# Performance work log

Hardware: AMD Instinct MI355X
Metric: run time of the kernel (lower is better)

The kernel has to match this reference:

```python
import jax, jax.numpy as jnp
import numpy as np

N_NODES = 50000
N_EDGES = 800000
N_GRAPHS = 64
IN_DIM, HID, OUT = 128, 128, 16


def gcn_conv(x, src, dst, deg_inv_sqrt, W, b):
    # x: [N, Cin]; src/dst: [E+N] (self-loops appended); W: [Cin, Cout]
    h = x @ W                                   # [N, Cout]
    norm = deg_inv_sqrt[src] * deg_inv_sqrt[dst]  # [E+N]
    msg = h[src] * norm[:, None]                # gather + scale
    out = jax.ops.segment_sum(msg, dst, num_segments=N_NODES)
    return out + b


def setup_inputs() -> dict:
    key = jax.random.key(0)
    ks = jax.random.split(key, 8)
    x = jax.random.normal(ks[0], (N_NODES, IN_DIM), dtype=jnp.float32)
    edge_index = jax.random.randint(ks[1], (2, N_EDGES), 0, N_NODES, dtype=jnp.int64)
    batch = jnp.sort(jax.random.randint(ks[2], (N_NODES,), 0, N_GRAPHS, dtype=jnp.int64))
    s = 1.0 / np.sqrt(IN_DIM)
    W1 = jax.random.normal(ks[3], (IN_DIM, HID), dtype=jnp.float32) * s
    b1 = jnp.zeros((HID,), dtype=jnp.float32)
    W2 = jax.random.normal(ks[4], (HID, HID), dtype=jnp.float32) * (1.0 / np.sqrt(HID))
    b2 = jnp.zeros((HID,), dtype=jnp.float32)
    Wfc = jax.random.normal(ks[5], (HID, OUT), dtype=jnp.float32) * (1.0 / np.sqrt(HID))
    bfc = jnp.zeros((OUT,), dtype=jnp.float32)
    return {"x": x, "edge_index": edge_index, "batch": batch,
            "W1": W1, "b1": b1, "W2": W2, "b2": b2, "Wfc": Wfc, "bfc": bfc}


def reference(x, edge_index, batch, W1, b1, W2, b2, Wfc, bfc):
    self_loops = jnp.arange(N_NODES, dtype=edge_index.dtype)
    src = jnp.concatenate([edge_index[0], self_loops])  # [E+N]
    dst = jnp.concatenate([edge_index[1], self_loops])
    deg = jax.ops.segment_sum(jnp.ones_like(dst, dtype=x.dtype), dst, num_segments=N_NODES)
    deg_inv_sqrt = jnp.where(deg > 0, jax.lax.rsqrt(deg), 0.0)

    h = jax.nn.relu(gcn_conv(x, src, dst, deg_inv_sqrt, W1, b1))
    h = jax.nn.relu(gcn_conv(h, src, dst, deg_inv_sqrt, W2, b2))

    # global mean pool over graphs
    sums = jax.ops.segment_sum(h, batch, num_segments=N_GRAPHS)         # [G, HID]
    cnts = jax.ops.segment_sum(jnp.ones((N_NODES,), h.dtype), batch, num_segments=N_GRAPHS)
    pooled = sums / jnp.maximum(cnts, 1.0)[:, None]

    return pooled @ Wfc + bfc  # [G, OUT]
```

## Files before the change

kernel.cpp:

```cpp
#include <hip/hip_runtime.h>
#include <math.h>

#define N_NODES 50000
#define N_EDGES 800000
#define N_GRAPHS 64
#define DIM 128
#define OUTD 16
#define POOL_BLOCKS 1024

#define BSHIFT 8
#define BNODES 256
#define NBUCK ((N_NODES + BNODES - 1) / BNODES)
#define TILE 2048
#define RCAP 8192
#define BSLOT 4864
#define GEMMB 256
#define BIN_GRID ((N_EDGES + TILE - 1) / TILE)

typedef __attribute__((ext_vector_type(8))) short short8;
typedef __attribute__((ext_vector_type(4))) float f32x4;

static __device__ __forceinline__ unsigned short f2bf(float f) {
    unsigned u = __float_as_uint(f);
    u += 0x7fffu + ((u >> 16) & 1u);
    return (unsigned short)(u >> 16);
}
static __device__ __forceinline__ float bfl(unsigned u) {
    return __uint_as_float(u << 16);
}
static __device__ __forceinline__ float bfh(unsigned u) {
    return __uint_as_float(u & 0xffff0000u);
}
static __device__ __forceinline__ float b2f(unsigned short u) {
    return __uint_as_float((unsigned)u << 16);
}

__global__ __launch_bounds__(256) void k_init(int* __restrict__ bcnt,
                                              float* __restrict__ pool,
                                              float* __restrict__ pcnt) {
    int tid = threadIdx.x;
    if (tid < NBUCK) bcnt[tid] = 0;
    for (int i = tid; i < N_GRAPHS * DIM; i += 256) pool[i] = 0.f;
    if (tid < N_GRAPHS) pcnt[tid] = 0.f;
}

template <int BF16IN>
static __device__ __forceinline__ void gemm_body(const void* __restrict__ Av,
                                                 const float* __restrict__ Wg,
                                                 unsigned short* __restrict__ C,
                                                 int nrows,
                                                 unsigned* smemW, unsigned* smemC,
                                                 int tile0, int tstride) {
    unsigned* Wl = smemW;
    {
        int t = threadIdx.x;
        int p = t & 63;
        int kp = p * 2;
        int n0 = (t >> 6) * 32;
        int kstep = kp >> 5;
        int quad = (kp >> 3) & 3;
        int jw = (kp & 7) >> 1;
        const float* r0 = Wg + (size_t)kp * DIM;
        const float* r1 = r0 + DIM;
        int rot = (p >> 2) & 7;
#pragma unroll
        for (int i4 = 0; i4 < 8; ++i4) {
            int nb = ((i4 + rot) & 7) * 4;
            int n = n0 + nb;
            float4 lo = *(const float4*)(r0 + n);
            float4 hi = *(const float4*)(r1 + n);
            const float* lp = &lo.x;
            const float* hp = &hi.x;
#pragma unroll
            for (int ii = 0; ii < 4; ++ii) {
                int nn = n + ii;
                int ct = nn >> 4;
                int l  = quad * 16 + (nn & 15);
                unsigned vlo = f2bf(lp[ii]);
                unsigned vhi = f2bf(hp[ii]);
                Wl[(((kstep * 8 + ct) * 64) + l) * 4 + jw] = vlo | (vhi << 16);
            }
        }
    }
    __syncthreads();

    int wid  = threadIdx.x >> 6;
    int lane = threadIdx.x & 63;
    int m    = lane & 15;
    int quad = lane >> 4;
    const short8* Wf = (const short8*)Wl;
    unsigned short* cs = (unsigned short*)smemC + wid * 4352;
    const unsigned char* cb = (const unsigned char*)smemC + wid * 8704;

    int ntiles = (nrows + 127) / 128;
    for (int tile = tile0; tile < ntiles; tile += tstride) {
        int row0 = tile * 128 + wid * 32;
        if (row0 >= nrows) continue;

        int rA = row0 + m;      if (rA >= nrows) rA = nrows - 1;
        int rB = row0 + 16 + m; if (rB >= nrows) rB = nrows - 1;

        short8 af0[4], af1[4];
        if (BF16IN) {
            const unsigned short* arowA = (const unsigned short*)Av + (size_t)rA * DIM + quad * 8;
            const unsigned short* arowB = (const unsigned short*)Av + (size_t)rB * DIM + quad * 8;
#pragma unroll
            for (int ks = 0; ks < 4; ++ks) {
                af0[ks] = *(const short8*)(arowA + ks * 32);
                af1[ks] = *(const short8*)(arowB + ks * 32);
            }
        } else {
            const float* arowA = (const float*)Av + (size_t)rA * DIM + quad * 8;
            const float* arowB = (const float*)Av + (size_t)rB * DIM + quad * 8;
#pragma unroll
            for (int ks = 0; ks < 4; ++ks) {
                float4 lo = *(const float4*)(arowA + ks * 32);
                float4 hi = *(const float4*)(arowA + ks * 32 + 4);
                short8 f;
                f[0] = (short)f2bf(lo.x); f[1] = (short)f2bf(lo.y);
                f[2] = (short)f2bf(lo.z); f[3] = (short)f2bf(lo.w);
                f[4] = (short)f2bf(hi.x); f[5] = (short)f2bf(hi.y);
                f[6] = (short)f2bf(hi.z); f[7] = (short)f2bf(hi.w);
                af0[ks] = f;
                lo = *(const float4*)(arowB + ks * 32);
                hi = *(const float4*)(arowB + ks * 32 + 4);
                f[0] = (short)f2bf(lo.x); f[1] = (short)f2bf(lo.y);
                f[2] = (short)f2bf(lo.z); f[3] = (short)f2bf(lo.w);
                f[4] = (short)f2bf(hi.x); f[5] = (short)f2bf(hi.y);
                f[6] = (short)f2bf(hi.z); f[7] = (short)f2bf(hi.w);
                af1[ks] = f;
            }
        }

        f32x4 acc0[8], acc1[8];
#pragma unroll
        for (int ct = 0; ct < 8; ++ct) {
            acc0[ct] = (f32x4){0.f, 0.f, 0.f, 0.f};
            acc1[ct] = (f32x4){0.f, 0.f, 0.f, 0.f};
        }

#pragma unroll
        for (int ks = 0; ks < 4; ++ks) {
#pragma unroll
            for (int ct = 0; ct < 8; ++ct) {
                short8 bfrag = Wf[(ks * 8 + ct) * 64 + lane];
                acc0[ct] = __builtin_amdgcn_mfma_f32_16x16x32_bf16(af0[ks], bfrag, acc0[ct], 0, 0, 0);
                acc1[ct] = __builtin_amdgcn_mfma_f32_16x16x32_bf16(af1[ks], bfrag, acc1[ct], 0, 0, 0);
            }
        }

#pragma unroll
        for (int ct = 0; ct < 8; ++ct) {
#pragma unroll
            for (int reg = 0; reg < 4; ++reg) {
                cs[(quad * 4 + reg) * 136 + ct * 16 + m]      = f2bf(acc0[ct][reg]);
                cs[(16 + quad * 4 + reg) * 136 + ct * 16 + m] = f2bf(acc1[ct][reg]);
            }
        }
#pragma unroll
        for (int i = 0; i < 8; ++i) {
            int rg = i * 4 + quad;
            int r = row0 + rg;
            if (r < nrows) {
                uint4 vv = *(const uint4*)(cb + rg * 272 + m * 16);
                *((uint4*)(C + (size_t)r * DIM) + m) = vv;
            }
        }
    }
}

__global__ __launch_bounds__(256) void k_fused1(const float* __restrict__ A,
                                                const float* __restrict__ Wg,
                                                unsigned short* __restrict__ C,
                                                int nrows,
                                                const int* __restrict__ src,
                                                const int* __restrict__ dstp,
                                                int* __restrict__ bcnt,
                                                unsigned* __restrict__ bucket_arr) {
    __shared__ unsigned smemW[32768 / 4];
    __shared__ unsigned smemC[34816 / 4];
    if (blockIdx.x >= GEMMB) {
        int* cnt  = (int*)smemW;
        int* base = cnt + NBUCK;
        int tile0 = (blockIdx.x - GEMMB) * TILE;
        for (int i = threadIdx.x; i < NBUCK; i += 256) cnt[i] = 0;
        __syncthreads();
#pragma unroll
        for (int j = 0; j < TILE / 512; ++j) {
            int e = tile0 + j * 512 + threadIdx.x * 2;
            if (e < N_EDGES) {
                int2 d = *(const int2*)(dstp + e);
                atomicAdd(&cnt[d.x >> BSHIFT], 1);
                atomicAdd(&cnt[d.y >> BSHIFT], 1);
            }
        }
        __syncthreads();
        for (int i = threadIdx.x; i < NBUCK; i += 256) {
            int c = cnt[i];
            base[i] = i * BSLOT + (c ? atomicAdd(&bcnt[i], c) : 0);
            cnt[i] = 0;
        }
        __syncthreads();
#pragma unroll
        for (int j = 0; j < TILE / 512; ++j) {
            int e = tile0 + j * 512 + threadIdx.x * 2;
            if (e < N_EDGES) {
                int2 s = *(const int2*)(src + e);
                int2 d = *(const int2*)(dstp + e);
                int b0 = d.x >> BSHIFT, b1 = d.y >> BSHIFT;
                int p0 = base[b0] + atomicAdd(&cnt[b0], 1);
                bucket_arr[p0] = (unsigned)s.x | ((unsigned)(d.x & 255) << 16);
                int p1 = base[b1] + atomicAdd(&cnt[b1], 1);
                bucket_arr[p1] = (unsigned)s.y | ((unsigned)(d.y & 255) << 16);
            }
        }
        return;
    }
    gemm_body<0>(A, Wg, C, nrows, smemW, smemC, blockIdx.x, GEMMB);
}

__global__ __launch_bounds__(256) void k_gemm2(const unsigned short* __restrict__ A,
                                               const float* __restrict__ Wg,
                                               unsigned short* __restrict__ C,
                                               int nrows) {
    __shared__ unsigned smemW[32768 / 4];
    __shared__ unsigned smemC[34816 / 4];
    gemm_body<1>(A, Wg, C, nrows, smemW, smemC, blockIdx.x, gridDim.x);
}

__global__ __launch_bounds__(256) void k_binB(const unsigned* __restrict__ barr,
                                              const int* __restrict__ bcnt,
                                              int* __restrict__ row_off,
                                              float* __restrict__ dis,
                                              unsigned short* __restrict__ csr) {
    __shared__ unsigned raw[RCAP];
    __shared__ unsigned short stage[RCAP];
    __shared__ int hist[BNODES];
    __shared__ int scn[BNODES];
    __shared__ int borig[256], bscan[256];
    int tid = threadIdx.x;
    int b = blockIdx.x;
    int n0 = b << BSHIFT;

    int cv = (tid < NBUCK) ? bcnt[tid] : 0;
    borig[tid] = cv;
    bscan[tid] = cv;
    __syncthreads();
    for (int off = 1; off < 256; off <<= 1) {
        int t = (tid >= off) ? bscan[tid - off] : 0;
        __syncthreads();
        bscan[tid] += t;
        __syncthreads();
    }
    int rbase = bscan[b] - borig[b];
    int len = borig[b];
    const unsigned* bin = barr + (size_t)b * BSLOT;

    hist[tid] = 0;
    __syncthreads();
    for (int i = tid; i < len; i += 256) {
        unsigned ed = bin[i];
        if (i < RCAP) raw[i] = ed;
        atomicAdd(&hist[ed >> 16], 1);
    }
    __syncthreads();
    int v = hist[tid];
    scn[tid] = v;
    __syncthreads();
    for (int off = 1; off < 256; off <<= 1) {
        int t = (tid >= off) ? scn[tid - off] : 0;
        __syncthreads();
        scn[tid] += t;
        __syncthreads();
    }
    int excl = scn[tid] - v;
    int n = n0 + tid;
    if (n < N_NODES) {
        row_off[n] = rbase + excl;
        dis[n] = rsqrtf((float)(v + 1));
    }
    if (b == NBUCK - 1 && tid == 0) row_off[N_NODES] = N_EDGES;
    hist[tid] = excl;
    __syncthreads();
    for (int i = tid; i < len; i += 256) {
        unsigned ed = (i < RCAP) ? raw[i] : bin[i];
        int p = atomicAdd(&hist[ed >> 16], 1);
        unsigned short sv = (unsigned short)(ed & 0xffffu);
        if (p < RCAP) stage[p] = sv;
        else csr[rbase + p] = sv;
    }
    __syncthreads();
    int lim = min(len, RCAP);
    for (int i = tid; i < lim; i += 256)
        csr[rbase + i] = stage[i];
}

__global__ __launch_bounds__(256) void k_agg(const uint4* __restrict__ Hb4,
                                             const int* __restrict__ row_off,
                                             const unsigned short* __restrict__ csr,
                                             const float* __restrict__ dis,
                                             const float* __restrict__ bias,
                                             uint4* __restrict__ out) {
    int lane = threadIdx.x & 15;
    int node = blockIdx.x * 16 + (threadIdx.x >> 4);
    if (node >= N_NODES) return;

    float dn = dis[node];
    float wself = dn * dn;
    uint4 hp = Hb4[(size_t)node * 16 + lane];
    float a0[8], a1[8], a2[8], a3[8];
    a0[0] = wself * bfl(hp.x); a0[1] = wself * bfh(hp.x);
    a0[2] = wself * bfl(hp.y); a0[3] = wself * bfh(hp.y);
    a0[4] = wself * bfl(hp.z); a0[5] = wself * bfh(hp.z);
    a0[6] = wself * bfl(hp.w); a0[7] = wself * bfh(hp.w);
#pragma unroll
    for (int j = 0; j < 8; ++j) { a1[j] = 0.f; a2[j] = 0.f; a3[j] = 0.f; }

    int e = row_off[node], e1 = row_off[node + 1];
    for (; e + 4 <= e1; e += 4) {
        int s0 = csr[e];     int s1 = csr[e + 1];
        int s2 = csr[e + 2]; int s3 = csr[e + 3];
        uint4 g0 = Hb4[(size_t)s0 * 16 + lane];
        uint4 g1 = Hb4[(size_t)s1 * 16 + lane];
        uint4 g2 = Hb4[(size_t)s2 * 16 + lane];
        uint4 g3 = Hb4[(size_t)s3 * 16 + lane];
        float w0 = dn * dis[s0], w1 = dn * dis[s1];
        float w2 = dn * dis[s2], w3 = dn * dis[s3];
        a0[0] = fmaf(w0, bfl(g0.x), a0[0]); a0[1] = fmaf(w0, bfh(g0.x), a0[1]);
        a0[2] = fmaf(w0, bfl(g0.y), a0[2]); a0[3] = fmaf(w0, bfh(g0.y), a0[3]);
        a0[4] = fmaf(w0, bfl(g0.z), a0[4]); a0[5] = fmaf(w0, bfh(g0.z), a0[5]);
        a0[6] = fmaf(w0, bfl(g0.w), a0[6]); a0[7] = fmaf(w0, bfh(g0.w), a0[7]);
        a1[0] = fmaf(w1, bfl(g1.x), a1[0]); a1[1] = fmaf(w1, bfh(g1.x), a1[1]);
        a1[2] = fmaf(w1, bfl(g1.y), a1[2]); a1[3] = fmaf(w1, bfh(g1.y), a1[3]);
        a1[4] = fmaf(w1, bfl(g1.z), a1[4]); a1[5] = fmaf(w1, bfh(g1.z), a1[5]);
        a1[6] = fmaf(w1, bfl(g1.w), a1[6]); a1[7] = fmaf(w1, bfh(g1.w), a1[7]);
        a2[0] = fmaf(w2, bfl(g2.x), a2[0]); a2[1] = fmaf(w2, bfh(g2.x), a2[1]);
        a2[2] = fmaf(w2, bfl(g2.y), a2[2]); a2[3] = fmaf(w2, bfh(g2.y), a2[3]);
        a2[4] = fmaf(w2, bfl(g2.z), a2[4]); a2[5] = fmaf(w2, bfh(g2.z), a2[5]);
        a2[6] = fmaf(w2, bfl(g2.w), a2[6]); a2[7] = fmaf(w2, bfh(g2.w), a2[7]);
        a3[0] = fmaf(w3, bfl(g3.x), a3[0]); a3[1] = fmaf(w3, bfh(g3.x), a3[1]);
        a3[2] = fmaf(w3, bfl(g3.y), a3[2]); a3[3] = fmaf(w3, bfh(g3.y), a3[3]);
        a3[4] = fmaf(w3, bfl(g3.z), a3[4]); a3[5] = fmaf(w3, bfh(g3.z), a3[5]);
        a3[6] = fmaf(w3, bfl(g3.w), a3[6]); a3[7] = fmaf(w3, bfh(g3.w), a3[7]);
    }
    for (; e < e1; ++e) {
        int s = csr[e];
        uint4 g = Hb4[(size_t)s * 16 + lane];
        float w = dn * dis[s];
        a0[0] = fmaf(w, bfl(g.x), a0[0]); a0[1] = fmaf(w, bfh(g.x), a0[1]);
        a0[2] = fmaf(w, bfl(g.y), a0[2]); a0[3] = fmaf(w, bfh(g.y), a0[3]);
        a0[4] = fmaf(w, bfl(g.z), a0[4]); a0[5] = fmaf(w, bfh(g.z), a0[5]);
        a0[6] = fmaf(w, bfl(g.w), a0[6]); a0[7] = fmaf(w, bfh(g.w), a0[7]);
    }

    float4 b0 = ((const float4*)bias)[lane * 2];
    float4 b1v = ((const float4*)bias)[lane * 2 + 1];
    float r[8];
    r[0] = fmaxf(a0[0] + a1[0] + a2[0] + a3[0] + b0.x, 0.f);
    r[1] = fmaxf(a0[1] + a1[1] + a2[1] + a3[1] + b0.y, 0.f);
    r[2] = fmaxf(a0[2] + a1[2] + a2[2] + a3[2] + b0.z, 0.f);
    r[3] = fmaxf(a0[3] + a1[3] + a2[3] + a3[3] + b0.w, 0.f);
    r[4] = fmaxf(a0[4] + a1[4] + a2[4] + a3[4] + b1v.x, 0.f);
    r[5] = fmaxf(a0[5] + a1[5] + a2[5] + a3[5] + b1v.y, 0.f);
    r[6] = fmaxf(a0[6] + a1[6] + a2[6] + a3[6] + b1v.z, 0.f);
    r[7] = fmaxf(a0[7] + a1[7] + a2[7] + a3[7] + b1v.w, 0.f);
    uint4 ov;
    ov.x = (unsigned)f2bf(r[0]) | ((unsigned)f2bf(r[1]) << 16);
    ov.y = (unsigned)f2bf(r[2]) | ((unsigned)f2bf(r[3]) << 16);
    ov.z = (unsigned)f2bf(r[4]) | ((unsigned)f2bf(r[5]) << 16);
    ov.w = (unsigned)f2bf(r[6]) | ((unsigned)f2bf(r[7]) << 16);
    out[(size_t)node * 16 + lane] = ov;
}

__global__ __launch_bounds__(128) void k_pool(const unsigned short* __restrict__ h,
                                              const int* __restrict__ batch,
                                              float* __restrict__ pool,
                                              float* __restrict__ pcnt) {
    int chunk = (N_NODES + POOL_BLOCKS - 1) / POOL_BLOCKS;
    int n0 = blockIdx.x * chunk;
    int n1 = min(n0 + chunk, N_NODES);
    if (n0 >= n1) return;
    int c = threadIdx.x;
    int curg = batch[n0];
    float acc = 0.f;
    int count = 0;
    int n = n0;
    for (; n + 4 <= n1; ) {
        int g0 = batch[n], g3 = batch[n + 3];
        if (g0 == curg && g3 == curg) {
            float v0 = b2f(h[(size_t)(n + 0) * DIM + c]);
            float v1 = b2f(h[(size_t)(n + 1) * DIM + c]);
            float v2 = b2f(h[(size_t)(n + 2) * DIM + c]);
            float v3 = b2f(h[(size_t)(n + 3) * DIM + c]);
            acc += (v0 + v1) + (v2 + v3);
            count += 4;
            n += 4;
        } else {
            int g = g0;
            if (g != curg) {
                atomicAdd(&pool[curg * DIM + c], acc);
                if (c == 0) atomicAdd(&pcnt[curg], (float)count);
                acc = 0.f; count = 0; curg = g;
            }
            acc += b2f(h[(size_t)n * DIM + c]);
            count++;
            n += 1;
        }
    }
    for (; n < n1; ++n) {
        int g = batch[n];
        if (g != curg) {
            atomicAdd(&pool[curg * DIM + c], acc);
            if (c == 0) atomicAdd(&pcnt[curg], (float)count);
            acc = 0.f; count = 0; curg = g;
        }
        acc += b2f(h[(size_t)n * DIM + c]);
        count++;
    }
    atomicAdd(&pool[curg * DIM + c], acc);
    if (c == 0) atomicAdd(&pcnt[curg], (float)count);
}

__global__ void k_fc(const float* __restrict__ pool, const float* __restrict__ pcnt,
                     const float* __restrict__ Wfc, const float* __restrict__ bfc,
                     float* __restrict__ out) {
    int id = blockIdx.x * blockDim.x + threadIdx.x;
    if (id >= N_GRAPHS * OUTD) return;
    int g = id >> 4, o = id & 15;
    float inv = 1.0f / fmaxf(pcnt[g], 1.0f);
    float acc = bfc[o];
    const float* p = pool + g * DIM;
    for (int c = 0; c < DIM; ++c)
        acc = fmaf(p[c] * inv, Wfc[c * OUTD + o], acc);
    out[id] = acc;
}


extern "C" void kernel_launch(void* const* d_in, const int* in_sizes, int n_in,
                              void* d_out, int out_size, void* d_ws, size_t ws_size,
                              hipStream_t stream) {
    const float* x    = (const float*)d_in[0];
    const int*   ei   = (const int*)d_in[1];
    const int*   batch= (const int*)d_in[2];
    const float* W1   = (const float*)d_in[3];
    const float* b1   = (const float*)d_in[4];
    const float* W2   = (const float*)d_in[5];
    const float* b2   = (const float*)d_in[6];
    const float* Wfc  = (const float*)d_in[7];
    const float* bfc  = (const float*)d_in[8];
    float* out = (float*)d_out;

    char* ws = (char*)d_ws;
    size_t off = 0;
    auto alloc = [&](size_t bytes) -> char* {
        char* p = ws + off;
        off = (off + bytes + 255) & ~(size_t)255;
        return p;
    };
    int*      bcnt     = (int*)     alloc((size_t)NBUCK * 4);
    int*      row_off  = (int*)     alloc((size_t)(N_NODES + 1) * 4);
    float*    dis      = (float*)   alloc((size_t)N_NODES * 4);
    unsigned short* csr= (unsigned short*)alloc((size_t)N_EDGES * 2);
    unsigned* barr     = (unsigned*)alloc((size_t)NBUCK * BSLOT * 4);
    float*    pool     = (float*)   alloc((size_t)N_GRAPHS * DIM * 4);
    float*    pcnt     = (float*)   alloc((size_t)N_GRAPHS * 4);
    unsigned short* Hb = (unsigned short*)alloc((size_t)N_NODES * DIM * 2);
    unsigned short* Hb2= (unsigned short*)alloc((size_t)N_NODES * DIM * 2);

    const int* src = ei;
    const int* dst = ei + N_EDGES;

    k_init<<<1, 256, 0, stream>>>(bcnt, pool, pcnt);
    k_fused1<<<GEMMB + BIN_GRID, 256, 0, stream>>>(x, W1, Hb, N_NODES,
                                                   src, dst, bcnt, barr);
    k_binB<<<NBUCK, 256, 0, stream>>>(barr, bcnt, row_off, dis, csr);

    int agg_grid = (N_NODES + 15) / 16;
    k_agg<<<agg_grid, 256, 0, stream>>>((const uint4*)Hb, row_off, csr, dis, b1, (uint4*)Hb2);
    k_gemm2<<<GEMMB, 256, 0, stream>>>(Hb2, W2, Hb, N_NODES);
    k_agg<<<agg_grid, 256, 0, stream>>>((const uint4*)Hb, row_off, csr, dis, b2, (uint4*)Hb2);
    k_pool<<<POOL_BLOCKS, DIM, 0, stream>>>(Hb2, batch, pool, pcnt);
    k_fc<<<(N_GRAPHS * OUTD + 255) / 256, 256, 0, stream>>>(pool, pcnt, Wfc, bfc, out);
}
```

Before: 207.9 us.

## Fuse global mean pooling into second aggregation and derive graph counts by binary search

The second aggregation kernel now reduces each block's 16 node rows in shared memory, per graph id. It then atomically adds the partial sums into the pooled buffer, instead of writing the bf16 hidden state and running a separate pool kernel. Per-graph node counts are now computed in the final FC kernel by binary search over the sorted batch array, which removes the count atomics and the count buffer. This avoids a full write and re-read of the second-layer activations and one kernel launch. In exchange there are many more global float atomics on the small pool buffer, and a block-level barrier in the aggregation kernel.

```diff
diff --git a/kernel.cpp b/kernel.cpp
--- a/kernel.cpp
+++ b/kernel.cpp
@@ -6,7 +6,6 @@
 #define N_GRAPHS 64
 #define DIM 128
 #define OUTD 16
-#define POOL_BLOCKS 1024
 
 #define BSHIFT 8
 #define BNODES 256
@@ -31,17 +30,12 @@
 static __device__ __forceinline__ float bfh(unsigned u) {
     return __uint_as_float(u & 0xffff0000u);
 }
-static __device__ __forceinline__ float b2f(unsigned short u) {
-    return __uint_as_float((unsigned)u << 16);
-}
 
 __global__ __launch_bounds__(256) void k_init(int* __restrict__ bcnt,
-                                              float* __restrict__ pool,
-                                              float* __restrict__ pcnt) {
+                                              float* __restrict__ pool) {
     int tid = threadIdx.x;
     if (tid < NBUCK) bcnt[tid] = 0;
     for (int i = tid; i < N_GRAPHS * DIM; i += 256) pool[i] = 0.f;
-    if (tid < N_GRAPHS) pcnt[tid] = 0.f;
 }
 
 template <int BF16IN>
@@ -295,14 +289,20 @@
         csr[rbase + i] = stage[i];
 }
 
+template <int FUSE_POOL>
 __global__ __launch_bounds__(256) void k_agg(const uint4* __restrict__ Hb4,
                                              const int* __restrict__ row_off,
                                              const unsigned short* __restrict__ csr,
                                              const float* __restrict__ dis,
                                              const float* __restrict__ bias,
-                                             uint4* __restrict__ out) {
+                                             uint4* __restrict__ out,
+                                             const int* __restrict__ batch,
+                                             float* __restrict__ pool) {
+    __shared__ float sacc[16][DIM];
+    __shared__ int sg[16];
     int lane = threadIdx.x & 15;
-    int node = blockIdx.x * 16 + (threadIdx.x >> 4);
+    int nl   = threadIdx.x >> 4;
+    int node = blockIdx.x * 16 + nl;
     if (node >= N_NODES) return;
 
     float dn = dis[node];
@@ -364,70 +364,50 @@
     r[5] = fmaxf(a0[5] + a1[5] + a2[5] + a3[5] + b1v.y, 0.f);
     r[6] = fmaxf(a0[6] + a1[6] + a2[6] + a3[6] + b1v.z, 0.f);
     r[7] = fmaxf(a0[7] + a1[7] + a2[7] + a3[7] + b1v.w, 0.f);
-    uint4 ov;
-    ov.x = (unsigned)f2bf(r[0]) | ((unsigned)f2bf(r[1]) << 16);
-    ov.y = (unsigned)f2bf(r[2]) | ((unsigned)f2bf(r[3]) << 16);
-    ov.z = (unsigned)f2bf(r[4]) | ((unsigned)f2bf(r[5]) << 16);
-    ov.w = (unsigned)f2bf(r[6]) | ((unsigned)f2bf(r[7]) << 16);
-    out[(size_t)node * 16 + lane] = ov;
-}
-
-__global__ __launch_bounds__(128) void k_pool(const unsigned short* __restrict__ h,
-                                              const int* __restrict__ batch,
-                                              float* __restrict__ pool,
-                                              float* __restrict__ pcnt) {
-    int chunk = (N_NODES + POOL_BLOCKS - 1) / POOL_BLOCKS;
-    int n0 = blockIdx.x * chunk;
-    int n1 = min(n0 + chunk, N_NODES);
-    if (n0 >= n1) return;
-    int c = threadIdx.x;
-    int curg = batch[n0];
-    float acc = 0.f;
-    int count = 0;
-    int n = n0;
-    for (; n + 4 <= n1; ) {
-        int g0 = batch[n], g3 = batch[n + 3];
-        if (g0 == curg && g3 == curg) {
-            float v0 = b2f(h[(size_t)(n + 0) * DIM + c]);
-            float v1 = b2f(h[(size_t)(n + 1) * DIM + c]);
-            float v2 = b2f(h[(size_t)(n + 2) * DIM + c]);
-            float v3 = b2f(h[(size_t)(n + 3) * DIM + c]);
-            acc += (v0 + v1) + (v2 + v3);
-            count += 4;
-            n += 4;
-        } else {
-            int g = g0;
-            if (g != curg) {
-                atomicAdd(&pool[curg * DIM + c], acc);
-                if (c == 0) atomicAdd(&pcnt[curg], (float)count);
-                acc = 0.f; count = 0; curg = g;
-            }
-            acc += b2f(h[(size_t)n * DIM + c]);
-            count++;
-            n += 1;
-        }
-    }
-    for (; n < n1; ++n) {
-        int g = batch[n];
-        if (g != curg) {
+
+    if (!FUSE_POOL) {
+        uint4 ov;
+        ov.x = (unsigned)f2bf(r[0]) | ((unsigned)f2bf(r[1]) << 16);
+        ov.y = (unsigned)f2bf(r[2]) | ((unsigned)f2bf(r[3]) << 16);
+        ov.z = (unsigned)f2bf(r[4]) | ((unsigned)f2bf(r[5]) << 16);
+        ov.w = (unsigned)f2bf(r[6]) | ((unsigned)f2bf(r[7]) << 16);
+        out[(size_t)node * 16 + lane] = ov;
+    } else {
+#pragma unroll
+        for (int j = 0; j < 8; ++j) sacc[nl][lane * 8 + j] = r[j];
+        if (lane == 0) sg[nl] = batch[node];
+        __syncthreads();
+        int c = threadIdx.x;
+        if (c < DIM) {
+            float acc = 0.f;
+            int curg = sg[0];
+#pragma unroll
+            for (int n = 0; n < 16; ++n) {
+                int g = sg[n];
+                if (g != curg) {
+                    atomicAdd(&pool[curg * DIM + c], acc);
+                    acc = 0.f; curg = g;
+                }
+                acc += sacc[n][c];
+            }
             atomicAdd(&pool[curg * DIM + c], acc);
-            if (c == 0) atomicAdd(&pcnt[curg], (float)count);
-            acc = 0.f; count = 0; curg = g;
-        }
-        acc += b2f(h[(size_t)n * DIM + c]);
-        count++;
-    }
-    atomicAdd(&pool[curg * DIM + c], acc);
-    if (c == 0) atomicAdd(&pcnt[curg], (float)count);
-}
-
-__global__ void k_fc(const float* __restrict__ pool, const float* __restrict__ pcnt,
+        }
+    }
+}
+
+__global__ void k_fc(const float* __restrict__ pool, const int* __restrict__ batch,
                      const float* __restrict__ Wfc, const float* __restrict__ bfc,
                      float* __restrict__ out) {
     int id = blockIdx.x * blockDim.x + threadIdx.x;
     if (id >= N_GRAPHS * OUTD) return;
     int g = id >> 4, o = id & 15;
-    float inv = 1.0f / fmaxf(pcnt[g], 1.0f);
+    int lo = 0, hi = N_NODES;
+    while (lo < hi) { int mid = (lo + hi) >> 1; if (batch[mid] < g) lo = mid + 1; else hi = mid; }
+    int l0 = lo;
+    lo = 0; hi = N_NODES;
+    while (lo < hi) { int mid = (lo + hi) >> 1; if (batch[mid] < g + 1) lo = mid + 1; else hi = mid; }
+    int cntg = lo - l0;
+    float inv = 1.0f / fmaxf((float)cntg, 1.0f);
     float acc = bfc[o];
     const float* p = pool + g * DIM;
     for (int c = 0; c < DIM; ++c)
@@ -463,22 +443,22 @@
     unsigned short* csr= (unsigned short*)alloc((size_t)N_EDGES * 2);
     unsigned* barr     = (unsigned*)alloc((size_t)NBUCK * BSLOT * 4);
     float*    pool     = (float*)   alloc((size_t)N_GRAPHS * DIM * 4);
-    float*    pcnt     = (float*)   alloc((size_t)N_GRAPHS * 4);
     unsigned short* Hb = (unsigned short*)alloc((size_t)N_NODES * DIM * 2);
     unsigned short* Hb2= (unsigned short*)alloc((size_t)N_NODES * DIM * 2);
 
     const int* src = ei;
     const int* dst = ei + N_EDGES;
 
-    k_init<<<1, 256, 0, stream>>>(bcnt, pool, pcnt);
+    k_init<<<1, 256, 0, stream>>>(bcnt, pool);
     k_fused1<<<GEMMB + BIN_GRID, 256, 0, stream>>>(x, W1, Hb, N_NODES,
                                                    src, dst, bcnt, barr);
     k_binB<<<NBUCK, 256, 0, stream>>>(barr, bcnt, row_off, dis, csr);
 
     int agg_grid = (N_NODES + 15) / 16;
-    k_agg<<<agg_grid, 256, 0, stream>>>((const uint4*)Hb, row_off, csr, dis, b1, (uint4*)Hb2);
+    k_agg<0><<<agg_grid, 256, 0, stream>>>((const uint4*)Hb, row_off, csr, dis, b1,
+                                           (uint4*)Hb2, batch, pool);
     k_gemm2<<<GEMMB, 256, 0, stream>>>(Hb2, W2, Hb, N_NODES);
-    k_agg<<<agg_grid, 256, 0, stream>>>((const uint4*)Hb, row_off, csr, dis, b2, (uint4*)Hb2);
-    k_pool<<<POOL_BLOCKS, DIM, 0, stream>>>(Hb2, batch, pool, pcnt);
-    k_fc<<<(N_GRAPHS * OUTD + 255) / 256, 256, 0, stream>>>(pool, pcnt, Wfc, bfc, out);
-}
+    k_agg<1><<<agg_grid, 256, 0, stream>>>((const uint4*)Hb, row_off, csr, dis, b2,
+                                           nullptr, batch, pool);
+    k_fc<<<(N_GRAPHS * OUTD + 255) / 256, 256, 0, stream>>>(pool, batch, Wfc, bfc, out);
+}
```

Measured after the change: 203.9 us. Within noise of the previous version (-1.9%).
